# Optimization experiments

Hardware: AMD Instinct MI355X
Metric: run time of the kernel (lower is better)

The kernel has to match this reference:

```python
import jax, jax.numpy as jnp
import numpy as np

N = 100_000   # nodes
E = 1_600_000 # edges (avg degree 16)
F_IN, H1, H2, H3, C = 32, 32, 32, 16, 8


def _gcn_conv(h, W, b, src, dst, norm):
    # h: [N, Fin] -> project then normalized sparse aggregate (PyG GCNConv)
    h = h @ W                                   # [N, Fout]
    msg = h[src] * norm[:, None]                # gather + scale, [E', Fout]
    agg = jax.ops.segment_sum(msg, dst, num_segments=N)
    return agg + b


def setup_inputs() -> dict:
    key = jax.random.key(0)
    ks = jax.random.split(key, 8)
    x = jax.random.normal(ks[0], (N, F_IN), dtype=jnp.float32)
    edge_index = jax.random.randint(ks[1], (2, E), 0, N, dtype=jnp.int64)
    def w(k, fi, fo):
        return jax.random.normal(k, (fi, fo), dtype=jnp.float32) / np.float32(np.sqrt(fi))
    return {
        "x": x,
        "edge_index": edge_index,
        "W1": w(ks[2], F_IN, H1), "b1": jnp.zeros((H1,), jnp.float32),
        "W2": w(ks[3], H1, H2),   "b2": jnp.zeros((H2,), jnp.float32),
        "W3": w(ks[4], H2, H3),   "b3": jnp.zeros((H3,), jnp.float32),
        "Wc": w(ks[5], H3, C),    "bc": jnp.zeros((C,), jnp.float32),
    }


def reference(x, edge_index, W1, b1, W2, b2, W3, b3, Wc, bc):
    src, dst = edge_index[0], edge_index[1]
    loops = jnp.arange(N, dtype=src.dtype)
    src_f = jnp.concatenate([src, loops])       # add self-loops
    dst_f = jnp.concatenate([dst, loops])
    # symmetric normalization D^-1/2 (A+I) D^-1/2 (deg over targets, incl. self-loop)
    deg = jax.ops.segment_sum(jnp.ones_like(dst_f, dtype=x.dtype), dst_f, num_segments=N)
    dinv = jax.lax.rsqrt(deg)                   # deg >= 1 due to self-loops
    norm = dinv[src_f] * dinv[dst_f]            # [E+N]

    h = jnp.tanh(_gcn_conv(x, W1, b1, src_f, dst_f, norm))
    h = jnp.tanh(_gcn_conv(h, W2, b2, src_f, dst_f, norm))
    h = jnp.tanh(_gcn_conv(h, W3, b3, src_f, dst_f, norm))
    out = h @ Wc + bc
    return (out, h)
```

## Files before the change

### kernel.cpp

```cpp
#include <hip/hip_runtime.h>

static constexpr int NN = 100000;
static constexpr int NE = 1600000;

static constexpr int BSH   = 9;
static constexpr int NDB   = 1 << BSH;
static constexpr int NBUCK = (NN + NDB - 1) / NDB;
static constexpr int BCAP  = 9216;
static constexpr int HSTRIDE = 8704;
static constexpr int BSTRIDE = 2 * HSTRIDE;
static constexpr int TILE  = 4096;
static constexpr int NBIN  = (NE + TILE - 1) / TILE;
static constexpr int EPT   = TILE / 256;

static_assert(NBUCK <= 256, "bucket count must fit one block");

__global__ __launch_bounds__(256) void k_bin_proj(const int* __restrict__ src,
                                                  const int* __restrict__ dst,
                                                  int* __restrict__ gcur,
                                                  unsigned* __restrict__ bkt,
                                                  const float* __restrict__ x,
                                                  const float* __restrict__ W1,
                                                  float* __restrict__ p) {
    const int t = threadIdx.x;
    if (blockIdx.x < NBIN) {
        __shared__ int hist[NBUCK];
        __shared__ int cur[NBUCK];
        const int e0 = blockIdx.x * TILE;
        const int n = (NE - e0 < TILE) ? (NE - e0) : TILE;
        for (int i = t; i < NBUCK; i += 256) hist[i] = 0;
        __syncthreads();
        unsigned rec[EPT];
        int bb[EPT];
#pragma unroll
        for (int j = 0; j < EPT; ++j) {
            const int i = t + j * 256;
            bb[j] = -1;
            if (i < n) {
                const int s = src[e0 + i];
                const int d = dst[e0 + i];
                bb[j] = d >> BSH;
                rec[j] = ((unsigned)s << BSH) | (unsigned)(d & (NDB - 1));
                atomicAdd(&hist[bb[j]], 1);
            }
        }
        __syncthreads();
        for (int i = t; i < NBUCK; i += 256) {
            const int c = hist[i];
            cur[i] = (c > 0) ? (i * BCAP + atomicAdd(&gcur[i], c)) : 0;
        }
        __syncthreads();
#pragma unroll
        for (int j = 0; j < EPT; ++j) {
            if (bb[j] >= 0) {
                const int pos = atomicAdd(&cur[bb[j]], 1);
                bkt[pos] = rec[j];
            }
        }
    } else {
        __shared__ float Ws[1024];
        __shared__ float rows[8][33];
        const int pb = blockIdx.x - NBIN;
        if (pb == 0 && t < 32) p[(size_t)NN * 32 + t] = 0.f;
        for (int i = t; i < 1024; i += 256) Ws[i] = W1[i];
        const int nl = t >> 5;
        const int f = t & 31;
        const int node = pb * 8 + nl;
        rows[nl][f] = x[(size_t)node * 32 + f];
        __syncthreads();
        float acc = 0.f;
#pragma unroll
        for (int k = 0; k < 32; ++k) acc += rows[nl][k] * Ws[k * 32 + f];
        p[(size_t)node * 32 + f] = acc;
    }
}

__global__ __launch_bounds__(256) void k_build(const unsigned* __restrict__ bkt,
                                               const int* __restrict__ gcur,
                                               int* __restrict__ csr,
                                               int* __restrict__ npad,
                                               int* __restrict__ offs,
                                               float* __restrict__ dinv,
                                               float* __restrict__ B0) {
    __shared__ int hist[256];
    __shared__ int sc[256];
    __shared__ int cur[256];
    const int bb = blockIdx.x;
    const int b = bb >> 1;
    const unsigned half = bb & 1;
    const int h0 = (b << BSH) + (int)half * 256;
    const int nh = (NN - h0 < 256) ? (NN - h0) : 256;
    const int t = threadIdx.x;
    int cnt = gcur[b];
    if (cnt > BCAP) cnt = BCAP;
    hist[t] = 0;
    __syncthreads();
    const unsigned* bp = bkt + (size_t)b * BCAP;
    if (nh > 0) {
        for (int i = t; i < cnt; i += 256) {
            const unsigned r = bp[i];
            if (((r >> 8) & 1u) == half) atomicAdd(&hist[r & 255], 1);
        }
    }
    __syncthreads();
    const int h = hist[t];
    const int lp = (h + 15) & ~15;
    sc[t] = lp;
    __syncthreads();
    for (int off = 1; off < 256; off <<= 1) {
        const int a = (t >= off) ? sc[t - off] : 0;
        __syncthreads();
        sc[t] += a;
        __syncthreads();
    }
    const int rbase = b * BSTRIDE + (int)half * HSTRIDE;
    const int e = rbase + (sc[t] - lp);
    cur[t] = e;
    if (t < nh) {
        const int node = h0 + t;
        npad[node] = lp;
        offs[node] = e;
        dinv[node] = rsqrtf((float)h + 1.0f);
        for (int j = h; j < lp; ++j) csr[e + j] = NN;
    }
    __syncthreads();
    if (nh > 0) {
        for (int i = t; i < cnt; i += 256) {
            const unsigned r = bp[i];
            if (((r >> 8) & 1u) == half) {
                const int pos = atomicAdd(&cur[r & 255], 1);
                csr[pos] = (int)(r >> BSH);
            }
        }
        float4* B04 = (float4*)B0;
        for (int i = t; i < nh * 8; i += 256) {
            const int node = h0 + (i >> 3);
            const float di = dinv[node];
            float4 v = B04[(size_t)node * 8 + (i & 7)];
            v.x *= di; v.y *= di; v.z *= di; v.w *= di;
            B04[(size_t)node * 8 + (i & 7)] = v;
        }
    }
}

template <int FOUT>
__global__ __launch_bounds__(256) void k_agg_proj(const float4* __restrict__ p4,
                                                  const int* __restrict__ offs,
                                                  const int* __restrict__ npad,
                                                  const float* __restrict__ dinv,
                                                  const int* __restrict__ csr,
                                                  const float4* __restrict__ bias4,
                                                  const float* __restrict__ W,
                                                  float* __restrict__ pout) {
    constexpr int NPB = 32;
    constexpr int OPL = FOUT / 8;
    __shared__ float Ws[32 * FOUT];
    __shared__ float hs[NPB][33];
    const int tid = threadIdx.x;
    if (blockIdx.x == 0 && tid < FOUT) pout[(size_t)NN * FOUT + tid] = 0.f;
    for (int i = tid; i < 32 * FOUT; i += 256) Ws[i] = W[i];
    const int nl = tid >> 3;
    const int f4 = tid & 7;
    const int node = blockIdx.x * NPB + nl;
    const int start = offs[node];
    const int L = npad[node];
    const float4 self = p4[(size_t)node * 8 + f4];
    float ax = self.x, ay = self.y, az = self.z, aw = self.w;
    for (int kk = 0; kk < L; kk += 16) {
        const int* cp = csr + start + kk;
        int s[16];
#pragma unroll
        for (int j = 0; j < 16; ++j) s[j] = cp[j];
        float4 v[16];
#pragma unroll
        for (int j = 0; j < 16; ++j) v[j] = p4[(size_t)s[j] * 8 + f4];
        float sx0 = 0.f, sy0 = 0.f, sz0 = 0.f, sw0 = 0.f;
        float sx1 = 0.f, sy1 = 0.f, sz1 = 0.f, sw1 = 0.f;
#pragma unroll
        for (int j = 0; j < 8; ++j) {
            sx0 += v[j].x; sy0 += v[j].y; sz0 += v[j].z; sw0 += v[j].w;
            sx1 += v[j + 8].x; sy1 += v[j + 8].y; sz1 += v[j + 8].z; sw1 += v[j + 8].w;
        }
        ax += sx0 + sx1; ay += sy0 + sy1; az += sz0 + sz1; aw += sw0 + sw1;
    }
    const float di = dinv[node];
    const float4 bb = bias4[f4];
    hs[nl][4 * f4 + 0] = tanhf(di * ax + bb.x);
    hs[nl][4 * f4 + 1] = tanhf(di * ay + bb.y);
    hs[nl][4 * f4 + 2] = tanhf(di * az + bb.z);
    hs[nl][4 * f4 + 3] = tanhf(di * aw + bb.w);
    __syncthreads();
    float acc[OPL];
#pragma unroll
    for (int o = 0; o < OPL; ++o) acc[o] = 0.f;
#pragma unroll
    for (int k = 0; k < 32; ++k) {
        const float hv = hs[nl][k];
#pragma unroll
        for (int o = 0; o < OPL; ++o) acc[o] += hv * Ws[k * FOUT + f4 * OPL + o];
    }
    if (OPL == 4) {
        float4 r;
        r.x = acc[0] * di; r.y = acc[1] * di; r.z = acc[2] * di; r.w = acc[OPL - 1] * di;
        reinterpret_cast<float4*>(pout)[(size_t)node * 8 + f4] = r;
    } else {
        float2 r;
        r.x = acc[0] * di; r.y = acc[OPL - 1] * di;
        reinterpret_cast<float2*>(pout)[(size_t)node * 8 + f4] = r;
    }
}

__global__ __launch_bounds__(256) void k_agg_cls(const float4* __restrict__ p4,
                                                 const int* __restrict__ offs,
                                                 const int* __restrict__ npad,
                                                 const float* __restrict__ dinv,
                                                 const int* __restrict__ csr,
                                                 const float4* __restrict__ bias4,
                                                 const float* __restrict__ Wc,
                                                 const float* __restrict__ bc,
                                                 float4* __restrict__ h4out,
                                                 float* __restrict__ out) {
    constexpr int NPB = 64;
    __shared__ float WcS[16 * 8];
    __shared__ float bcS[8];
    __shared__ float hs[NPB][17];
    const int tid = threadIdx.x;
    if (tid < 128) WcS[tid] = Wc[tid];
    if (tid < 8) bcS[tid] = bc[tid];
    const int nl = tid >> 2;
    const int f4 = tid & 3;
    int node = blockIdx.x * NPB + nl;
    if (node >= NN) node = NN - 1;
    const int start = offs[node];
    const int L = npad[node];
    const float4 self = p4[(size_t)node * 4 + f4];
    float ax = self.x, ay = self.y, az = self.z, aw = self.w;
    for (int kk = 0; kk < L; kk += 16) {
        const int* cp = csr + start + kk;
        int s[16];
#pragma unroll
        for (int j = 0; j < 16; ++j) s[j] = cp[j];
        float4 v[16];
#pragma unroll
        for (int j = 0; j < 16; ++j) v[j] = p4[(size_t)s[j] * 4 + f4];
        float sx0 = 0.f, sy0 = 0.f, sz0 = 0.f, sw0 = 0.f;
        float sx1 = 0.f, sy1 = 0.f, sz1 = 0.f, sw1 = 0.f;
#pragma unroll
        for (int j = 0; j < 8; ++j) {
            sx0 += v[j].x; sy0 += v[j].y; sz0 += v[j].z; sw0 += v[j].w;
            sx1 += v[j + 8].x; sy1 += v[j + 8].y; sz1 += v[j + 8].z; sw1 += v[j + 8].w;
        }
        ax += sx0 + sx1; ay += sy0 + sy1; az += sz0 + sz1; aw += sw0 + sw1;
    }
    const float di = dinv[node];
    const float4 bb = bias4[f4];
    float4 h;
    h.x = tanhf(di * ax + bb.x);
    h.y = tanhf(di * ay + bb.y);
    h.z = tanhf(di * az + bb.z);
    h.w = tanhf(di * aw + bb.w);
    h4out[(size_t)node * 4 + f4] = h;
    hs[nl][4 * f4 + 0] = h.x;
    hs[nl][4 * f4 + 1] = h.y;
    hs[nl][4 * f4 + 2] = h.z;
    hs[nl][4 * f4 + 3] = h.w;
    __syncthreads();
    float a0 = bcS[2 * f4], a1 = bcS[2 * f4 + 1];
#pragma unroll
    for (int k = 0; k < 16; ++k) {
        const float hv = hs[nl][k];
        a0 += hv * WcS[k * 8 + 2 * f4];
        a1 += hv * WcS[k * 8 + 2 * f4 + 1];
    }
    reinterpret_cast<float2*>(out)[(size_t)node * 4 + f4] = make_float2(a0, a1);
}


extern "C" void kernel_launch(void* const* d_in, const int* in_sizes, int n_in,
                              void* d_out, int out_size, void* d_ws, size_t ws_size,
                              hipStream_t stream) {
    const float* x  = (const float*)d_in[0];
    const int*   ei = (const int*)d_in[1];
    const float* W1 = (const float*)d_in[2];
    const float* b1 = (const float*)d_in[3];
    const float* W2 = (const float*)d_in[4];
    const float* b2 = (const float*)d_in[5];
    const float* W3 = (const float*)d_in[6];
    const float* b3 = (const float*)d_in[7];
    const float* Wc = (const float*)d_in[8];
    const float* bc = (const float*)d_in[9];

    const int* src = ei;
    const int* dst = ei + NE;

    int*   gcur = (int*)d_ws;
    int*   npad = gcur + 256;
    int*   offs = npad + NN;
    float* dinv = (float*)(offs + NN);
    int*   csr  = (int*)(dinv + NN);
    float* B0   = (float*)(csr + (size_t)NBUCK * BSTRIDE);
    float* B1   = B0 + (size_t)(NN + 1) * 32;
    unsigned* bkt = (unsigned*)B1;

    float* out = (float*)d_out;
    float* h3  = out + (size_t)NN * 8;

    const int T = 256;

    hipMemsetAsync(gcur, 0, NBUCK * sizeof(int), stream);

    k_bin_proj<<<NBIN + NN / 8, T, 0, stream>>>(src, dst, gcur, bkt, x, W1, B0);

    k_build<<<2 * NBUCK, T, 0, stream>>>(bkt, gcur, csr, npad, offs, dinv, B0);

    k_agg_proj<32><<<NN / 32, T, 0, stream>>>((const float4*)B0, offs, npad, dinv, csr,
                                              (const float4*)b1, W2, B1);

    k_agg_proj<16><<<NN / 32, T, 0, stream>>>((const float4*)B1, offs, npad, dinv, csr,
                                              (const float4*)b2, W3, B0);

    k_agg_cls<<<(NN + 63) / 64, T, 0, stream>>>((const float4*)B0, offs, npad, dinv, csr,
                                                (const float4*)b3, Wc, bc,
                                                (float4*)h3, out);
}
```

Baseline: 151.7 us.

## Store intermediate node features in fp16 and pad neighbor lists to 8

The projected node features exchanged between layers move from fp32 to packed fp16, so each gathered neighbor row costs half the bytes, and accumulation still happens in fp32. Neighbor lists are now padded to multiples of 8 instead of 16, with a tail loop added to handle the last 8 entries, which cuts wasted padding gathers and shrinks the CSR stride. The projection kernel is reorganized to compute two outputs per thread and write them as half2. The risk is reduced accuracy in the intermediate features, which may fall outside the reference tolerance.

```diff
diff --git a/kernel.cpp b/kernel.cpp
--- a/kernel.cpp
+++ b/kernel.cpp
@@ -1,4 +1,5 @@
 #include <hip/hip_runtime.h>
+#include <hip/hip_fp16.h>
 
 static constexpr int NN = 100000;
 static constexpr int NE = 1600000;
@@ -7,13 +8,26 @@
 static constexpr int NDB   = 1 << BSH;
 static constexpr int NBUCK = (NN + NDB - 1) / NDB;
 static constexpr int BCAP  = 9216;
-static constexpr int HSTRIDE = 8704;
+static constexpr int HSTRIDE = 6656;
 static constexpr int BSTRIDE = 2 * HSTRIDE;
 static constexpr int TILE  = 4096;
 static constexpr int NBIN  = (NE + TILE - 1) / TILE;
 static constexpr int EPT   = TILE / 256;
 
 static_assert(NBUCK <= 256, "bucket count must fit one block");
+static_assert(NN % 32 == 0, "grids assume divisibility");
+
+__device__ __forceinline__ float4 h4tof4(uint2 r) {
+    const __half2 a = *reinterpret_cast<const __half2*>(&r.x);
+    const __half2 b = *reinterpret_cast<const __half2*>(&r.y);
+    const float2 fa = __half22float2(a);
+    const float2 fb = __half22float2(b);
+    return make_float4(fa.x, fa.y, fb.x, fb.y);
+}
+__device__ __forceinline__ unsigned packh2(float a, float b) {
+    __half2 h = __floats2half2_rn(a, b);
+    return *reinterpret_cast<unsigned*>(&h);
+}
 
 __global__ __launch_bounds__(256) void k_bin_proj(const int* __restrict__ src,
                                                   const int* __restrict__ dst,
@@ -21,7 +35,7 @@
                                                   unsigned* __restrict__ bkt,
                                                   const float* __restrict__ x,
                                                   const float* __restrict__ W1,
-                                                  float* __restrict__ p) {
+                                                  __half* __restrict__ p) {
     const int t = threadIdx.x;
     if (blockIdx.x < NBIN) {
         __shared__ int hist[NBUCK];
@@ -59,19 +73,25 @@
         }
     } else {
         __shared__ float Ws[1024];
-        __shared__ float rows[8][33];
+        __shared__ float xr[16][33];
         const int pb = blockIdx.x - NBIN;
-        if (pb == 0 && t < 32) p[(size_t)NN * 32 + t] = 0.f;
+        if (pb == 0 && t < 16) ((unsigned*)p)[(size_t)NN * 16 + t] = 0u;
         for (int i = t; i < 1024; i += 256) Ws[i] = W1[i];
-        const int nl = t >> 5;
-        const int f = t & 31;
-        const int node = pb * 8 + nl;
-        rows[nl][f] = x[(size_t)node * 32 + f];
-        __syncthreads();
-        float acc = 0.f;
-#pragma unroll
-        for (int k = 0; k < 32; ++k) acc += rows[nl][k] * Ws[k * 32 + f];
-        p[(size_t)node * 32 + f] = acc;
+        const int nl = t >> 4;
+        const int f2 = t & 15;
+        const int node = pb * 16 + nl;
+        const float2 xv = ((const float2*)x)[(size_t)node * 16 + f2];
+        xr[nl][2 * f2] = xv.x;
+        xr[nl][2 * f2 + 1] = xv.y;
+        __syncthreads();
+        float a0 = 0.f, a1 = 0.f;
+#pragma unroll
+        for (int k = 0; k < 32; ++k) {
+            const float hv = xr[nl][k];
+            a0 += hv * Ws[k * 32 + 2 * f2];
+            a1 += hv * Ws[k * 32 + 2 * f2 + 1];
+        }
+        ((unsigned*)p)[(size_t)node * 16 + f2] = packh2(a0, a1);
     }
 }
 
@@ -81,7 +101,7 @@
                                                int* __restrict__ npad,
                                                int* __restrict__ offs,
                                                float* __restrict__ dinv,
-                                               float* __restrict__ B0) {
+                                               __half* __restrict__ B0) {
     __shared__ int hist[256];
     __shared__ int sc[256];
     __shared__ int cur[256];
@@ -104,7 +124,7 @@
     }
     __syncthreads();
     const int h = hist[t];
-    const int lp = (h + 15) & ~15;
+    const int lp = (h + 7) & ~7;
     sc[t] = lp;
     __syncthreads();
     for (int off = 1; off < 256; off <<= 1) {
@@ -132,56 +152,74 @@
                 csr[pos] = (int)(r >> BSH);
             }
         }
-        float4* B04 = (float4*)B0;
-        for (int i = t; i < nh * 8; i += 256) {
-            const int node = h0 + (i >> 3);
+        unsigned* P = (unsigned*)B0;
+        for (int i = t; i < nh * 16; i += 256) {
+            const int node = h0 + (i >> 4);
             const float di = dinv[node];
-            float4 v = B04[(size_t)node * 8 + (i & 7)];
-            v.x *= di; v.y *= di; v.z *= di; v.w *= di;
-            B04[(size_t)node * 8 + (i & 7)] = v;
+            unsigned v = P[(size_t)node * 16 + (i & 15)];
+            float2 f = __half22float2(*reinterpret_cast<__half2*>(&v));
+            P[(size_t)node * 16 + (i & 15)] = packh2(f.x * di, f.y * di);
         }
     }
 }
 
 template <int FOUT>
-__global__ __launch_bounds__(256) void k_agg_proj(const float4* __restrict__ p4,
+__global__ __launch_bounds__(256) void k_agg_proj(const uint2* __restrict__ pu,
                                                   const int* __restrict__ offs,
                                                   const int* __restrict__ npad,
                                                   const float* __restrict__ dinv,
                                                   const int* __restrict__ csr,
                                                   const float4* __restrict__ bias4,
                                                   const float* __restrict__ W,
-                                                  float* __restrict__ pout) {
+                                                  __half* __restrict__ pout) {
     constexpr int NPB = 32;
     constexpr int OPL = FOUT / 8;
     __shared__ float Ws[32 * FOUT];
     __shared__ float hs[NPB][33];
     const int tid = threadIdx.x;
-    if (blockIdx.x == 0 && tid < FOUT) pout[(size_t)NN * FOUT + tid] = 0.f;
+    if (blockIdx.x == 0 && tid < FOUT / 2)
+        ((unsigned*)pout)[(size_t)NN * (FOUT / 2) + tid] = 0u;
     for (int i = tid; i < 32 * FOUT; i += 256) Ws[i] = W[i];
     const int nl = tid >> 3;
     const int f4 = tid & 7;
     const int node = blockIdx.x * NPB + nl;
     const int start = offs[node];
     const int L = npad[node];
-    const float4 self = p4[(size_t)node * 8 + f4];
+    const float4 self = h4tof4(pu[(size_t)node * 8 + f4]);
     float ax = self.x, ay = self.y, az = self.z, aw = self.w;
-    for (int kk = 0; kk < L; kk += 16) {
+    int kk = 0;
+    for (; kk + 16 <= L; kk += 16) {
         const int* cp = csr + start + kk;
         int s[16];
 #pragma unroll
         for (int j = 0; j < 16; ++j) s[j] = cp[j];
-        float4 v[16];
-#pragma unroll
-        for (int j = 0; j < 16; ++j) v[j] = p4[(size_t)s[j] * 8 + f4];
+        uint2 v[16];
+#pragma unroll
+        for (int j = 0; j < 16; ++j) v[j] = pu[(size_t)s[j] * 8 + f4];
         float sx0 = 0.f, sy0 = 0.f, sz0 = 0.f, sw0 = 0.f;
         float sx1 = 0.f, sy1 = 0.f, sz1 = 0.f, sw1 = 0.f;
 #pragma unroll
         for (int j = 0; j < 8; ++j) {
-            sx0 += v[j].x; sy0 += v[j].y; sz0 += v[j].z; sw0 += v[j].w;
-            sx1 += v[j + 8].x; sy1 += v[j + 8].y; sz1 += v[j + 8].z; sw1 += v[j + 8].w;
+            const float4 f0 = h4tof4(v[j]);
+            const float4 f1 = h4tof4(v[j + 8]);
+            sx0 += f0.x; sy0 += f0.y; sz0 += f0.z; sw0 += f0.w;
+            sx1 += f1.x; sy1 += f1.y; sz1 += f1.z; sw1 += f1.w;
         }
         ax += sx0 + sx1; ay += sy0 + sy1; az += sz0 + sz1; aw += sw0 + sw1;
+    }
+    if (kk < L) {
+        const int* cp = csr + start + kk;
+        int s[8];
+#pragma unroll
+        for (int j = 0; j < 8; ++j) s[j] = cp[j];
+        uint2 v[8];
+#pragma unroll
+        for (int j = 0; j < 8; ++j) v[j] = pu[(size_t)s[j] * 8 + f4];
+#pragma unroll
+        for (int j = 0; j < 8; ++j) {
+            const float4 f0 = h4tof4(v[j]);
+            ax += f0.x; ay += f0.y; az += f0.z; aw += f0.w;
+        }
     }
     const float di = dinv[node];
     const float4 bb = bias4[f4];
@@ -200,17 +238,16 @@
         for (int o = 0; o < OPL; ++o) acc[o] += hv * Ws[k * FOUT + f4 * OPL + o];
     }
     if (OPL == 4) {
-        float4 r;
-        r.x = acc[0] * di; r.y = acc[1] * di; r.z = acc[2] * di; r.w = acc[OPL - 1] * di;
-        reinterpret_cast<float4*>(pout)[(size_t)node * 8 + f4] = r;
+        uint2 r;
+        r.x = packh2(acc[0] * di, acc[1] * di);
+        r.y = packh2(acc[2] * di, acc[OPL - 1] * di);
+        ((uint2*)pout)[(size_t)node * 8 + f4] = r;
     } else {
-        float2 r;
-        r.x = acc[0] * di; r.y = acc[OPL - 1] * di;
-        reinterpret_cast<float2*>(pout)[(size_t)node * 8 + f4] = r;
-    }
-}
-
-__global__ __launch_bounds__(256) void k_agg_cls(const float4* __restrict__ p4,
+        ((unsigned*)pout)[(size_t)node * 8 + f4] = packh2(acc[0] * di, acc[OPL - 1] * di);
+    }
+}
+
+__global__ __launch_bounds__(256) void k_agg_cls(const uint2* __restrict__ pu,
                                                  const int* __restrict__ offs,
                                                  const int* __restrict__ npad,
                                                  const float* __restrict__ dinv,
@@ -233,24 +270,41 @@
     if (node >= NN) node = NN - 1;
     const int start = offs[node];
     const int L = npad[node];
-    const float4 self = p4[(size_t)node * 4 + f4];
+    const float4 self = h4tof4(pu[(size_t)node * 4 + f4]);
     float ax = self.x, ay = self.y, az = self.z, aw = self.w;
-    for (int kk = 0; kk < L; kk += 16) {
+    int kk = 0;
+    for (; kk + 16 <= L; kk += 16) {
         const int* cp = csr + start + kk;
         int s[16];
 #pragma unroll
         for (int j = 0; j < 16; ++j) s[j] = cp[j];
-        float4 v[16];
-#pragma unroll
-        for (int j = 0; j < 16; ++j) v[j] = p4[(size_t)s[j] * 4 + f4];
+        uint2 v[16];
+#pragma unroll
+        for (int j = 0; j < 16; ++j) v[j] = pu[(size_t)s[j] * 4 + f4];
         float sx0 = 0.f, sy0 = 0.f, sz0 = 0.f, sw0 = 0.f;
         float sx1 = 0.f, sy1 = 0.f, sz1 = 0.f, sw1 = 0.f;
 #pragma unroll
         for (int j = 0; j < 8; ++j) {
-            sx0 += v[j].x; sy0 += v[j].y; sz0 += v[j].z; sw0 += v[j].w;
-            sx1 += v[j + 8].x; sy1 += v[j + 8].y; sz1 += v[j + 8].z; sw1 += v[j + 8].w;
+            const float4 f0 = h4tof4(v[j]);
+            const float4 f1 = h4tof4(v[j + 8]);
+            sx0 += f0.x; sy0 += f0.y; sz0 += f0.z; sw0 += f0.w;
+            sx1 += f1.x; sy1 += f1.y; sz1 += f1.z; sw1 += f1.w;
         }
         ax += sx0 + sx1; ay += sy0 + sy1; az += sz0 + sz1; aw += sw0 + sw1;
+    }
+    if (kk < L) {
+        const int* cp = csr + start + kk;
+        int s[8];
+#pragma unroll
+        for (int j = 0; j < 8; ++j) s[j] = cp[j];
+        uint2 v[8];
+#pragma unroll
+        for (int j = 0; j < 8; ++j) v[j] = pu[(size_t)s[j] * 4 + f4];
+#pragma unroll
+        for (int j = 0; j < 8; ++j) {
+            const float4 f0 = h4tof4(v[j]);
+            ax += f0.x; ay += f0.y; az += f0.z; aw += f0.w;
+        }
     }
     const float di = dinv[node];
     const float4 bb = bias4[f4];
@@ -293,14 +347,14 @@
     const int* src = ei;
     const int* dst = ei + NE;
 
-    int*   gcur = (int*)d_ws;
-    int*   npad = gcur + 256;
-    int*   offs = npad + NN;
-    float* dinv = (float*)(offs + NN);
-    int*   csr  = (int*)(dinv + NN);
-    float* B0   = (float*)(csr + (size_t)NBUCK * BSTRIDE);
-    float* B1   = B0 + (size_t)(NN + 1) * 32;
-    unsigned* bkt = (unsigned*)B1;
+    int*    gcur = (int*)d_ws;
+    int*    npad = gcur + 256;
+    int*    offs = npad + NN;
+    float*  dinv = (float*)(offs + NN);
+    int*    csr  = (int*)(dinv + NN);
+    __half* B0   = (__half*)(csr + (size_t)NBUCK * BSTRIDE);
+    __half* B1   = B0 + (size_t)(NN + 1) * 32;
+    unsigned* bkt = (unsigned*)(B1 + (size_t)(NN + 1) * 32);
 
     float* out = (float*)d_out;
     float* h3  = out + (size_t)NN * 8;
@@ -309,17 +363,17 @@
 
     hipMemsetAsync(gcur, 0, NBUCK * sizeof(int), stream);
 
-    k_bin_proj<<<NBIN + NN / 8, T, 0, stream>>>(src, dst, gcur, bkt, x, W1, B0);
+    k_bin_proj<<<NBIN + NN / 16, T, 0, stream>>>(src, dst, gcur, bkt, x, W1, B0);
 
     k_build<<<2 * NBUCK, T, 0, stream>>>(bkt, gcur, csr, npad, offs, dinv, B0);
 
-    k_agg_proj<32><<<NN / 32, T, 0, stream>>>((const float4*)B0, offs, npad, dinv, csr,
+    k_agg_proj<32><<<NN / 32, T, 0, stream>>>((const uint2*)B0, offs, npad, dinv, csr,
                                               (const float4*)b1, W2, B1);
 
-    k_agg_proj<16><<<NN / 32, T, 0, stream>>>((const float4*)B1, offs, npad, dinv, csr,
+    k_agg_proj<16><<<NN / 32, T, 0, stream>>>((const uint2*)B1, offs, npad, dinv, csr,
                                               (const float4*)b2, W3, B0);
 
-    k_agg_cls<<<(NN + 63) / 64, T, 0, stream>>>((const float4*)B0, offs, npad, dinv, csr,
+    k_agg_cls<<<(NN + 63) / 64, T, 0, stream>>>((const uint2*)B0, offs, npad, dinv, csr,
                                                 (const float4*)b3, Wc, bc,
                                                 (float4*)h3, out);
 }
```

Result: faster. 134.5 us (-11.3%).
